# Optimization experiments

Hardware: AMD Instinct MI355X
Metric: run time of the kernel (lower is better)

The kernel has to match this reference:

```python
import jax, jax.numpy as jnp
import numpy as np

M_MARGIN = 0.5
S_SCALE = 30.0
EPS = 1e-12

def _l2norm(a):
    return a / jnp.maximum(jnp.linalg.norm(a, axis=1, keepdims=True), EPS)

def setup_inputs() -> dict:
    key = jax.random.key(0)
    k1, k2, k3 = jax.random.split(key, 3)
    B, D, V = 2048, 512, 32000
    x = jax.random.normal(k1, (B, D), dtype=jnp.float32)
    # kaiming_normal_ on (V, D): std = sqrt(2 / D)
    W = jax.random.normal(k2, (V, D), dtype=jnp.float32) * np.sqrt(2.0 / D)
    labels = jax.random.randint(k3, (B,), 0, V, dtype=jnp.int64)
    return {"x": x, "W": W, "labels": labels}

def reference(x, W, labels):
    cos_m, sin_m = jnp.cos(M_MARGIN), jnp.sin(M_MARGIN)
    nx = _l2norm(x)            # [B, D]
    nW = _l2norm(W)            # [V, D]
    cosine = nx @ nW.T         # [B, V]
    B = cosine.shape[0]
    rows = jnp.arange(B)
    # phi only matters at the label column (phi.where(one_hot, cosine))
    cos_y = cosine[rows, labels]                            # [B]
    sin_y = jnp.sqrt(jnp.clip(1.0 - cos_y * cos_y, 0.0, 1.0))
    phi_y = cos_y * cos_m - sin_y * sin_m                   # [B]
    logits = cosine.at[rows, labels].set(phi_y) * S_SCALE   # [B, V]
    logp = jax.nn.log_softmax(logits, axis=1)
    return -logp[rows, labels].sum() / B
```

## Files before the change

### kernel.cpp

```cpp
#include <hip/hip_runtime.h>
#include <math.h>
#include <stdint.h>

#define B_ROWS 2048
#define D_DIM  512
#define V_COLS 32000
#define BM 128
#define BN 128
#define BK 64
#define KSTEPS (D_DIM / BK)
#define NCT    (V_COLS / BN)
#define S_SC   30.0f
#define COS_M  0.8775825618903728f
#define SIN_M  0.479425538604203f

typedef float f32x4 __attribute__((ext_vector_type(4)));
typedef long  i64x2 __attribute__((ext_vector_type(2)));

__device__ __forceinline__ void load16_to_lds(const void* g, void* l) {
  __builtin_amdgcn_global_load_lds(
      (__attribute__((address_space(1))) void*)(g),
      (__attribute__((address_space(3))) void*)(l),
      16, 0, 0);
}

__global__ void fused_norm_kernel(const float* __restrict__ x,
                                  const float* __restrict__ W,
                                  uint8_t* __restrict__ nx,
                                  uint8_t* __restrict__ nw,
                                  float* __restrict__ rowsum,
                                  float* __restrict__ out) {
  if (blockIdx.x == 0 && threadIdx.x == 0) out[0] = 0.f;
  if (blockIdx.x < B_ROWS / 256) rowsum[blockIdx.x * 256 + threadIdx.x] = 0.f;
  const int lane = threadIdx.x & 63;
  const int wave = threadIdx.x >> 6;
  const int gr   = blockIdx.x * 4 + wave;
  const float* src;
  uint8_t* dst;
  if (gr < B_ROWS) {
    src = x + (size_t)gr * D_DIM;
    dst = nx + (size_t)gr * D_DIM;
  } else {
    src = W + (size_t)(gr - B_ROWS) * D_DIM;
    dst = nw + (size_t)(gr - B_ROWS) * D_DIM;
  }
  const float4* r4 = (const float4*)src;
  float4 v0 = r4[2 * lane];
  float4 v1 = r4[2 * lane + 1];
  float ss = v0.x*v0.x + v0.y*v0.y + v0.z*v0.z + v0.w*v0.w
           + v1.x*v1.x + v1.y*v1.y + v1.z*v1.z + v1.w*v1.w;
  #pragma unroll
  for (int off = 32; off >= 1; off >>= 1) ss += __shfl_xor(ss, off, 64);
  float inv = 1.0f / fmaxf(sqrtf(ss), 1e-12f);
  int p0 = __builtin_amdgcn_cvt_pk_fp8_f32(v0.x * inv, v0.y * inv, 0, false);
  p0     = __builtin_amdgcn_cvt_pk_fp8_f32(v0.z * inv, v0.w * inv, p0, true);
  int p1 = __builtin_amdgcn_cvt_pk_fp8_f32(v1.x * inv, v1.y * inv, 0, false);
  p1     = __builtin_amdgcn_cvt_pk_fp8_f32(v1.z * inv, v1.w * inv, p1, true);
  ((int2*)dst)[lane] = make_int2(p0, p1);
}

__global__ __launch_bounds__(256, 4)
void arc_gemm_kernel(const uint8_t* __restrict__ nx,
                     const uint8_t* __restrict__ nw,
                     const int* __restrict__ labels,
                     float* __restrict__ rowsum,
                     float* __restrict__ lbl_logit) {
  __shared__ uint8_t sA[2][BM * BK];
  __shared__ uint8_t sB[2][BN * BK];

  const int id = blockIdx.x;
  const int ct = ((id >> 7) << 3) | (id & 7);
  if (ct >= NCT) return;
  const int rt = (id >> 3) & 15;
  const int m0 = rt * BM;
  const int n0 = ct * BN;

  const int tid  = threadIdx.x;
  const int wave = tid >> 6;
  const int lane = tid & 63;
  const int wm   = wave >> 1;
  const int wn   = wave & 1;
  const int quad = lane >> 4;
  const int l16  = lane & 15;

  const int srow = tid >> 2;
  const int jg   = (tid & 3) ^ ((srow >> 1) & 3);
  const uint8_t* gA = nx + (size_t)(m0 + srow) * D_DIM + jg * 16;
  const uint8_t* gB = nw + (size_t)(n0 + srow) * D_DIM + jg * 16;
  const int ldsOff0 = wave * 1024;
  const int ldsOff1 = 4096 + wave * 1024;

  const int cSlot = (quad ^ ((l16 >> 1) & 3)) << 4;
  const int aBase = (wm * 64 + l16) * BK + cSlot;
  const int bBase = (wn * 64 + l16) * BK + cSlot;

  f32x4 acc[4][4];
  #pragma unroll
  for (int i = 0; i < 4; ++i)
    #pragma unroll
    for (int j = 0; j < 4; ++j) acc[i][j] = (f32x4){0.f, 0.f, 0.f, 0.f};

  load16_to_lds(gA,              &sA[0][ldsOff0]);
  load16_to_lds(gA + 64 * D_DIM, &sA[0][ldsOff1]);
  load16_to_lds(gB,              &sB[0][ldsOff0]);
  load16_to_lds(gB + 64 * D_DIM, &sB[0][ldsOff1]);

  #pragma unroll
  for (int ks = 0; ks < KSTEPS; ++ks) {
    __syncthreads();
    if (ks + 1 < KSTEPS) {
      const int off = (ks + 1) * BK;
      const int nb  = (ks + 1) & 1;
      load16_to_lds(gA + off,              &sA[nb][ldsOff0]);
      load16_to_lds(gA + 64 * D_DIM + off, &sA[nb][ldsOff1]);
      load16_to_lds(gB + off,              &sB[nb][ldsOff0]);
      load16_to_lds(gB + 64 * D_DIM + off, &sB[nb][ldsOff1]);
    }
    __syncthreads();

    const uint8_t* bA = sA[ks & 1];
    const uint8_t* bB = sB[ks & 1];
    i64x2 a2[4];
    #pragma unroll
    for (int mi = 0; mi < 4; ++mi)
      a2[mi] = *(const i64x2*)(bA + aBase + mi * 16 * BK);
    #pragma unroll
    for (int ni = 0; ni < 4; ++ni) {
      const i64x2 b2 = *(const i64x2*)(bB + bBase + ni * 16 * BK);
      #pragma unroll
      for (int mi = 0; mi < 4; ++mi) {
        acc[mi][ni] = __builtin_amdgcn_mfma_f32_16x16x32_fp8_fp8(a2[mi][0], b2[0], acc[mi][ni], 0, 0, 0);
        acc[mi][ni] = __builtin_amdgcn_mfma_f32_16x16x32_fp8_fp8(a2[mi][1], b2[1], acc[mi][ni], 0, 0, 0);
      }
    }
  }

  const int lblv = labels[m0 + wm * 64 + lane];
  #pragma unroll
  for (int mi = 0; mi < 4; ++mi) {
    #pragma unroll
    for (int r = 0; r < 4; ++r) {
      const int rw   = mi * 16 + quad * 4 + r;
      const int grow = m0 + wm * 64 + rw;
      const int lbl  = __shfl(lblv, rw, 64);
      float rsum = 0.f;
      #pragma unroll
      for (int ni = 0; ni < 4; ++ni) {
        float c = acc[mi][ni][r];
        const int gcol = n0 + wn * 64 + ni * 16 + l16;
        if (gcol == lbl) {
          float sy  = sqrtf(fminf(1.f, fmaxf(0.f, 1.f - c * c)));
          float phi = c * COS_M - sy * SIN_M;
          lbl_logit[grow] = S_SC * phi;
          c = phi;
        }
        rsum += __expf(S_SC * c - 30.0f);
      }
      #pragma unroll
      for (int off = 1; off < 16; off <<= 1)
        rsum += __shfl_xor(rsum, off, 64);
      if (l16 == 0) atomicAdd(&rowsum[grow], rsum);
    }
  }
}

__global__ void arc_finish_kernel(const float* __restrict__ rowsum,
                                  const float* __restrict__ lbl_logit,
                                  float* __restrict__ out) {
  const int row  = blockIdx.x * 256 + threadIdx.x;
  const int lane = threadIdx.x & 63;
  const int wave = threadIdx.x >> 6;
  float v = (30.0f + logf(rowsum[row]) - lbl_logit[row]) * (1.0f / (float)B_ROWS);
  #pragma unroll
  for (int off = 32; off >= 1; off >>= 1) v += __shfl_xor(v, off, 64);
  __shared__ float wsum[4];
  if (lane == 0) wsum[wave] = v;
  __syncthreads();
  if (threadIdx.x == 0) atomicAdd(out, wsum[0] + wsum[1] + wsum[2] + wsum[3]);
}

extern "C" void kernel_launch(void* const* d_in, const int* in_sizes, int n_in,
                              void* d_out, int out_size, void* d_ws, size_t ws_size,
                              hipStream_t stream) {
  const float* x      = (const float*)d_in[0];
  const float* W      = (const float*)d_in[1];
  const int*   labels = (const int*)d_in[2];
  float* out = (float*)d_out;

  char* ws = (char*)d_ws;
  uint8_t* nx = (uint8_t*)ws;
  uint8_t* nw = (uint8_t*)(ws + (size_t)B_ROWS * D_DIM);
  char* p = ws + (size_t)B_ROWS * D_DIM + (size_t)V_COLS * D_DIM;
  float* rowsum    = (float*)p;  p += (size_t)B_ROWS * 4;
  float* lbl_logit = (float*)p;

  hipLaunchKernelGGL(fused_norm_kernel, dim3((B_ROWS + V_COLS) / 4), dim3(256), 0, stream,
                     x, W, nx, nw, rowsum, out);
  hipLaunchKernelGGL(arc_gemm_kernel, dim3(32 * 16 * 8), dim3(256), 0, stream,
                     nx, nw, labels, rowsum, lbl_logit);
  hipLaunchKernelGGL(arc_finish_kernel, dim3(B_ROWS / 256), dim3(256), 0, stream,
                     rowsum, lbl_logit, out);
}
```

Measured before the change: 175.2 us.

## Enlarge GEMM tiles to 256x256 with 8 waves and triple-buffered LDS pipeline

Doubles the block tile to 256x256 with 512 threads (2x4 waves, each computing 128x64), which raises operand reuse per LDS byte. It replaces the double-buffer scheme, which had two barriers per k-step, with a three-stage buffer that uses explicit vmcnt waits and a single barrier, plus setprio around the MFMA block. Block-to-tile mapping is also remapped so that consecutive blocks share column tiles. The costs are higher register pressure (32 accumulators per wave), 96KB of LDS, and fewer blocks (1000), which risks worse tail balance across CUs.

```diff
diff --git a/kernel.cpp b/kernel.cpp
--- a/kernel.cpp
+++ b/kernel.cpp
@@ -5,10 +5,11 @@
 #define B_ROWS 2048
 #define D_DIM  512
 #define V_COLS 32000
-#define BM 128
-#define BN 128
+#define BM 256
+#define BN 256
 #define BK 64
 #define KSTEPS (D_DIM / BK)
+#define NRT    (B_ROWS / BM)
 #define NCT    (V_COLS / BN)
 #define S_SC   30.0f
 #define COS_M  0.8775825618903728f
@@ -59,27 +60,25 @@
   ((int2*)dst)[lane] = make_int2(p0, p1);
 }
 
-__global__ __launch_bounds__(256, 4)
+__global__ __launch_bounds__(512, 2)
 void arc_gemm_kernel(const uint8_t* __restrict__ nx,
                      const uint8_t* __restrict__ nw,
                      const int* __restrict__ labels,
                      float* __restrict__ rowsum,
                      float* __restrict__ lbl_logit) {
-  __shared__ uint8_t sA[2][BM * BK];
-  __shared__ uint8_t sB[2][BN * BK];
+  __shared__ uint8_t sA[3][BM * BK];
+  __shared__ uint8_t sB[3][BN * BK];
 
   const int id = blockIdx.x;
-  const int ct = ((id >> 7) << 3) | (id & 7);
-  if (ct >= NCT) return;
-  const int rt = (id >> 3) & 15;
-  const int m0 = rt * BM;
-  const int n0 = ct * BN;
+  const int wg = (id & 7) * NCT + (id >> 3);
+  const int m0 = (wg & (NRT - 1)) * BM;
+  const int n0 = (wg >> 3) * BN;
 
   const int tid  = threadIdx.x;
   const int wave = tid >> 6;
   const int lane = tid & 63;
-  const int wm   = wave >> 1;
-  const int wn   = wave & 1;
+  const int wm   = wave >> 2;
+  const int wn   = wave & 3;
   const int quad = lane >> 4;
   const int l16  = lane & 15;
 
@@ -87,62 +86,69 @@
   const int jg   = (tid & 3) ^ ((srow >> 1) & 3);
   const uint8_t* gA = nx + (size_t)(m0 + srow) * D_DIM + jg * 16;
   const uint8_t* gB = nw + (size_t)(n0 + srow) * D_DIM + jg * 16;
-  const int ldsOff0 = wave * 1024;
-  const int ldsOff1 = 4096 + wave * 1024;
+  const int ldsW = wave * 1024;
 
   const int cSlot = (quad ^ ((l16 >> 1) & 3)) << 4;
-  const int aBase = (wm * 64 + l16) * BK + cSlot;
-  const int bBase = (wn * 64 + l16) * BK + cSlot;
-
-  f32x4 acc[4][4];
-  #pragma unroll
-  for (int i = 0; i < 4; ++i)
+  const int aBase = (wm * 128 + l16) * BK + cSlot;
+  const int bBase = (wn * 64  + l16) * BK + cSlot;
+
+  f32x4 acc[8][4];
+  #pragma unroll
+  for (int i = 0; i < 8; ++i)
     #pragma unroll
     for (int j = 0; j < 4; ++j) acc[i][j] = (f32x4){0.f, 0.f, 0.f, 0.f};
 
-  load16_to_lds(gA,              &sA[0][ldsOff0]);
-  load16_to_lds(gA + 64 * D_DIM, &sA[0][ldsOff1]);
-  load16_to_lds(gB,              &sB[0][ldsOff0]);
-  load16_to_lds(gB + 64 * D_DIM, &sB[0][ldsOff1]);
-
-  #pragma unroll
-  for (int ks = 0; ks < KSTEPS; ++ks) {
-    __syncthreads();
-    if (ks + 1 < KSTEPS) {
-      const int off = (ks + 1) * BK;
-      const int nb  = (ks + 1) & 1;
-      load16_to_lds(gA + off,              &sA[nb][ldsOff0]);
-      load16_to_lds(gA + 64 * D_DIM + off, &sA[nb][ldsOff1]);
-      load16_to_lds(gB + off,              &sB[nb][ldsOff0]);
-      load16_to_lds(gB + 64 * D_DIM + off, &sB[nb][ldsOff1]);
-    }
-    __syncthreads();
-
-    const uint8_t* bA = sA[ks & 1];
-    const uint8_t* bB = sB[ks & 1];
-    i64x2 a2[4];
-    #pragma unroll
-    for (int mi = 0; mi < 4; ++mi)
-      a2[mi] = *(const i64x2*)(bA + aBase + mi * 16 * BK);
+#define STAGE(buf, t) do {                                        \
+    const int _o = (t) * BK;                                      \
+    load16_to_lds(gA + _o,               &sA[(buf)][ldsW]);       \
+    load16_to_lds(gA + 128 * D_DIM + _o, &sA[(buf)][8192 + ldsW]);\
+    load16_to_lds(gB + _o,               &sB[(buf)][ldsW]);       \
+    load16_to_lds(gB + 128 * D_DIM + _o, &sB[(buf)][8192 + ldsW]);\
+  } while (0)
+
+  STAGE(0, 0);
+  STAGE(1, 1);
+
+  #pragma unroll
+  for (int t = 0; t < KSTEPS; ++t) {
+    if (t < KSTEPS - 1) asm volatile("s_waitcnt vmcnt(4)" ::: "memory");
+    else                asm volatile("s_waitcnt vmcnt(0)" ::: "memory");
+    __builtin_amdgcn_s_barrier();
+    __builtin_amdgcn_sched_barrier(0);
+    if (t + 2 < KSTEPS) STAGE((t + 2) % 3, t + 2);
+    __builtin_amdgcn_sched_barrier(0);
+
+    const uint8_t* bA = sA[t % 3];
+    const uint8_t* bB = sB[t % 3];
+    i64x2 a2[8];
+    #pragma unroll
+    for (int mi = 0; mi < 8; ++mi)
+      a2[mi] = *(const i64x2*)(bA + aBase + mi * 1024);
+    __builtin_amdgcn_s_setprio(1);
     #pragma unroll
     for (int ni = 0; ni < 4; ++ni) {
-      const i64x2 b2 = *(const i64x2*)(bB + bBase + ni * 16 * BK);
+      const i64x2 b2 = *(const i64x2*)(bB + bBase + ni * 1024);
       #pragma unroll
-      for (int mi = 0; mi < 4; ++mi) {
+      for (int mi = 0; mi < 8; ++mi) {
         acc[mi][ni] = __builtin_amdgcn_mfma_f32_16x16x32_fp8_fp8(a2[mi][0], b2[0], acc[mi][ni], 0, 0, 0);
         acc[mi][ni] = __builtin_amdgcn_mfma_f32_16x16x32_fp8_fp8(a2[mi][1], b2[1], acc[mi][ni], 0, 0, 0);
       }
     }
+    __builtin_amdgcn_s_setprio(0);
   }
-
-  const int lblv = labels[m0 + wm * 64 + lane];
-  #pragma unroll
-  for (int mi = 0; mi < 4; ++mi) {
+#undef STAGE
+
+  const int rowbase = m0 + wm * 128;
+  const int lblv0 = labels[rowbase + lane];
+  const int lblv1 = labels[rowbase + 64 + lane];
+  #pragma unroll
+  for (int mi = 0; mi < 8; ++mi) {
     #pragma unroll
     for (int r = 0; r < 4; ++r) {
       const int rw   = mi * 16 + quad * 4 + r;
-      const int grow = m0 + wm * 64 + rw;
-      const int lbl  = __shfl(lblv, rw, 64);
+      const int grow = rowbase + rw;
+      const int lbl  = __shfl(mi < 4 ? lblv0 : lblv1,
+                              (mi & 3) * 16 + quad * 4 + r, 64);
       float rsum = 0.f;
       #pragma unroll
       for (int ni = 0; ni < 4; ++ni) {
@@ -196,7 +202,7 @@
 
   hipLaunchKernelGGL(fused_norm_kernel, dim3((B_ROWS + V_COLS) / 4), dim3(256), 0, stream,
                      x, W, nx, nw, rowsum, out);
-  hipLaunchKernelGGL(arc_gemm_kernel, dim3(32 * 16 * 8), dim3(256), 0, stream,
+  hipLaunchKernelGGL(arc_gemm_kernel, dim3(NRT * NCT), dim3(512), 0, stream,
                      nx, nw, labels, rowsum, lbl_logit);
   hipLaunchKernelGGL(arc_finish_kernel, dim3(B_ROWS / 256), dim3(256), 0, stream,
                      rowsum, lbl_logit, out);
```

Result: slower. 222.3 us (+26.9%).

## Fuse norm, GEMM and finish into one persistent cooperative kernel with grid syncs

Applied to the files above, without the earlier changes.

Replaces three kernel launches with a single cooperative persistent kernel of 512 blocks. Each block grid-strides over the normalization rows and over the GEMM tiles, with grid-wide barriers between the phases, and finishes with the loss reduction. This removes launch gaps and inter-kernel drain and fill. It adds grid-sync overhead and fixes the GEMM to 512 resident blocks, which may leave little latency hiding and cause tail imbalance over the 2000 tiles. The normalization load pattern also changes to coalesced float4 loads at lane and lane+64.

```diff
diff --git a/kernel.cpp b/kernel.cpp
--- a/kernel.cpp
+++ b/kernel.cpp
@@ -1,4 +1,5 @@
 #include <hip/hip_runtime.h>
+#include <hip/hip_cooperative_groups.h>
 #include <math.h>
 #include <stdint.h>
 
@@ -10,6 +11,8 @@
 #define BK 64
 #define KSTEPS (D_DIM / BK)
 #define NCT    (V_COLS / BN)
+#define GRID   512
+#define NIDS   4096
 #define S_SC   30.0f
 #define COS_M  0.8775825618903728f
 #define SIN_M  0.479425538604203f
@@ -24,159 +27,157 @@
       16, 0, 0);
 }
 
-__global__ void fused_norm_kernel(const float* __restrict__ x,
-                                  const float* __restrict__ W,
-                                  uint8_t* __restrict__ nx,
-                                  uint8_t* __restrict__ nw,
-                                  float* __restrict__ rowsum,
-                                  float* __restrict__ out) {
-  if (blockIdx.x == 0 && threadIdx.x == 0) out[0] = 0.f;
-  if (blockIdx.x < B_ROWS / 256) rowsum[blockIdx.x * 256 + threadIdx.x] = 0.f;
-  const int lane = threadIdx.x & 63;
-  const int wave = threadIdx.x >> 6;
-  const int gr   = blockIdx.x * 4 + wave;
-  const float* src;
-  uint8_t* dst;
-  if (gr < B_ROWS) {
-    src = x + (size_t)gr * D_DIM;
-    dst = nx + (size_t)gr * D_DIM;
-  } else {
-    src = W + (size_t)(gr - B_ROWS) * D_DIM;
-    dst = nw + (size_t)(gr - B_ROWS) * D_DIM;
-  }
-  const float4* r4 = (const float4*)src;
-  float4 v0 = r4[2 * lane];
-  float4 v1 = r4[2 * lane + 1];
-  float ss = v0.x*v0.x + v0.y*v0.y + v0.z*v0.z + v0.w*v0.w
-           + v1.x*v1.x + v1.y*v1.y + v1.z*v1.z + v1.w*v1.w;
-  #pragma unroll
-  for (int off = 32; off >= 1; off >>= 1) ss += __shfl_xor(ss, off, 64);
-  float inv = 1.0f / fmaxf(sqrtf(ss), 1e-12f);
-  int p0 = __builtin_amdgcn_cvt_pk_fp8_f32(v0.x * inv, v0.y * inv, 0, false);
-  p0     = __builtin_amdgcn_cvt_pk_fp8_f32(v0.z * inv, v0.w * inv, p0, true);
-  int p1 = __builtin_amdgcn_cvt_pk_fp8_f32(v1.x * inv, v1.y * inv, 0, false);
-  p1     = __builtin_amdgcn_cvt_pk_fp8_f32(v1.z * inv, v1.w * inv, p1, true);
-  ((int2*)dst)[lane] = make_int2(p0, p1);
-}
-
 __global__ __launch_bounds__(256, 4)
-void arc_gemm_kernel(const uint8_t* __restrict__ nx,
-                     const uint8_t* __restrict__ nw,
-                     const int* __restrict__ labels,
-                     float* __restrict__ rowsum,
-                     float* __restrict__ lbl_logit) {
+void arc_fused_kernel(const float* __restrict__ x,
+                      const float* __restrict__ W,
+                      const int* __restrict__ labels,
+                      uint8_t* __restrict__ nx,
+                      uint8_t* __restrict__ nw,
+                      float* __restrict__ rowsum,
+                      float* __restrict__ lbl_logit,
+                      float* __restrict__ out) {
   __shared__ uint8_t sA[2][BM * BK];
   __shared__ uint8_t sB[2][BN * BK];
 
-  const int id = blockIdx.x;
-  const int ct = ((id >> 7) << 3) | (id & 7);
-  if (ct >= NCT) return;
-  const int rt = (id >> 3) & 15;
-  const int m0 = rt * BM;
-  const int n0 = ct * BN;
-
   const int tid  = threadIdx.x;
+  const int lane = tid & 63;
   const int wave = tid >> 6;
-  const int lane = tid & 63;
+
+  if (blockIdx.x == 0 && tid == 0) out[0] = 0.f;
+  if (blockIdx.x < B_ROWS / 256) rowsum[blockIdx.x * 256 + tid] = 0.f;
+
+  for (int r = blockIdx.x * 4 + wave; r < B_ROWS + V_COLS; r += GRID * 4) {
+    const float* src;
+    uint8_t* dst;
+    if (r < B_ROWS) {
+      src = x + (size_t)r * D_DIM;
+      dst = nx + (size_t)r * D_DIM;
+    } else {
+      src = W + (size_t)(r - B_ROWS) * D_DIM;
+      dst = nw + (size_t)(r - B_ROWS) * D_DIM;
+    }
+    const float4* r4 = (const float4*)src;
+    float4 v0 = r4[lane];
+    float4 v1 = r4[lane + 64];
+    float ss = v0.x*v0.x + v0.y*v0.y + v0.z*v0.z + v0.w*v0.w
+             + v1.x*v1.x + v1.y*v1.y + v1.z*v1.z + v1.w*v1.w;
+    #pragma unroll
+    for (int off = 32; off >= 1; off >>= 1) ss += __shfl_xor(ss, off, 64);
+    float inv = 1.0f / fmaxf(sqrtf(ss), 1e-12f);
+    int p0 = __builtin_amdgcn_cvt_pk_fp8_f32(v0.x * inv, v0.y * inv, 0, false);
+    p0     = __builtin_amdgcn_cvt_pk_fp8_f32(v0.z * inv, v0.w * inv, p0, true);
+    int p1 = __builtin_amdgcn_cvt_pk_fp8_f32(v1.x * inv, v1.y * inv, 0, false);
+    p1     = __builtin_amdgcn_cvt_pk_fp8_f32(v1.z * inv, v1.w * inv, p1, true);
+    ((int*)dst)[lane]      = p0;
+    ((int*)dst)[64 + lane] = p1;
+  }
+
+  cooperative_groups::this_grid().sync();
+
   const int wm   = wave >> 1;
   const int wn   = wave & 1;
   const int quad = lane >> 4;
   const int l16  = lane & 15;
-
   const int srow = tid >> 2;
   const int jg   = (tid & 3) ^ ((srow >> 1) & 3);
-  const uint8_t* gA = nx + (size_t)(m0 + srow) * D_DIM + jg * 16;
-  const uint8_t* gB = nw + (size_t)(n0 + srow) * D_DIM + jg * 16;
   const int ldsOff0 = wave * 1024;
   const int ldsOff1 = 4096 + wave * 1024;
-
   const int cSlot = (quad ^ ((l16 >> 1) & 3)) << 4;
   const int aBase = (wm * 64 + l16) * BK + cSlot;
   const int bBase = (wn * 64 + l16) * BK + cSlot;
 
-  f32x4 acc[4][4];
-  #pragma unroll
-  for (int i = 0; i < 4; ++i)
-    #pragma unroll
-    for (int j = 0; j < 4; ++j) acc[i][j] = (f32x4){0.f, 0.f, 0.f, 0.f};
-
-  load16_to_lds(gA,              &sA[0][ldsOff0]);
-  load16_to_lds(gA + 64 * D_DIM, &sA[0][ldsOff1]);
-  load16_to_lds(gB,              &sB[0][ldsOff0]);
-  load16_to_lds(gB + 64 * D_DIM, &sB[0][ldsOff1]);
-
-  #pragma unroll
-  for (int ks = 0; ks < KSTEPS; ++ks) {
-    __syncthreads();
-    if (ks + 1 < KSTEPS) {
-      const int off = (ks + 1) * BK;
-      const int nb  = (ks + 1) & 1;
-      load16_to_lds(gA + off,              &sA[nb][ldsOff0]);
-      load16_to_lds(gA + 64 * D_DIM + off, &sA[nb][ldsOff1]);
-      load16_to_lds(gB + off,              &sB[nb][ldsOff0]);
-      load16_to_lds(gB + 64 * D_DIM + off, &sB[nb][ldsOff1]);
+  for (int v = blockIdx.x; v < NIDS; v += GRID) {
+    const int ct = ((v >> 7) << 3) | (v & 7);
+    if (ct >= NCT) continue;
+    const int rt = (v >> 3) & 15;
+    const int m0 = rt * BM;
+    const int n0 = ct * BN;
+
+    const uint8_t* gA = nx + (size_t)(m0 + srow) * D_DIM + jg * 16;
+    const uint8_t* gB = nw + (size_t)(n0 + srow) * D_DIM + jg * 16;
+
+    f32x4 acc[4][4];
+    #pragma unroll
+    for (int i = 0; i < 4; ++i)
+      #pragma unroll
+      for (int j = 0; j < 4; ++j) acc[i][j] = (f32x4){0.f, 0.f, 0.f, 0.f};
+
+    load16_to_lds(gA,              &sA[0][ldsOff0]);
+    load16_to_lds(gA + 64 * D_DIM, &sA[0][ldsOff1]);
+    load16_to_lds(gB,              &sB[0][ldsOff0]);
+    load16_to_lds(gB + 64 * D_DIM, &sB[0][ldsOff1]);
+
+    #pragma unroll
+    for (int ks = 0; ks < KSTEPS; ++ks) {
+      __syncthreads();
+      if (ks + 1 < KSTEPS) {
+        const int off = (ks + 1) * BK;
+        const int nb  = (ks + 1) & 1;
+        load16_to_lds(gA + off,              &sA[nb][ldsOff0]);
+        load16_to_lds(gA + 64 * D_DIM + off, &sA[nb][ldsOff1]);
+        load16_to_lds(gB + off,              &sB[nb][ldsOff0]);
+        load16_to_lds(gB + 64 * D_DIM + off, &sB[nb][ldsOff1]);
+      }
+      __syncthreads();
+
+      const uint8_t* bA = sA[ks & 1];
+      const uint8_t* bB = sB[ks & 1];
+      i64x2 a2[4];
+      #pragma unroll
+      for (int mi = 0; mi < 4; ++mi)
+        a2[mi] = *(const i64x2*)(bA + aBase + mi * 16 * BK);
+      #pragma unroll
+      for (int ni = 0; ni < 4; ++ni) {
+        const i64x2 b2 = *(const i64x2*)(bB + bBase + ni * 16 * BK);
+        #pragma unroll
+        for (int mi = 0; mi < 4; ++mi) {
+          acc[mi][ni] = __builtin_amdgcn_mfma_f32_16x16x32_fp8_fp8(a2[mi][0], b2[0], acc[mi][ni], 0, 0, 0);
+          acc[mi][ni] = __builtin_amdgcn_mfma_f32_16x16x32_fp8_fp8(a2[mi][1], b2[1], acc[mi][ni], 0, 0, 0);
+        }
+      }
     }
-    __syncthreads();
-
-    const uint8_t* bA = sA[ks & 1];
-    const uint8_t* bB = sB[ks & 1];
-    i64x2 a2[4];
-    #pragma unroll
-    for (int mi = 0; mi < 4; ++mi)
-      a2[mi] = *(const i64x2*)(bA + aBase + mi * 16 * BK);
-    #pragma unroll
-    for (int ni = 0; ni < 4; ++ni) {
-      const i64x2 b2 = *(const i64x2*)(bB + bBase + ni * 16 * BK);
-      #pragma unroll
-      for (int mi = 0; mi < 4; ++mi) {
-        acc[mi][ni] = __builtin_amdgcn_mfma_f32_16x16x32_fp8_fp8(a2[mi][0], b2[0], acc[mi][ni], 0, 0, 0);
-        acc[mi][ni] = __builtin_amdgcn_mfma_f32_16x16x32_fp8_fp8(a2[mi][1], b2[1], acc[mi][ni], 0, 0, 0);
+
+    const int lblv = labels[m0 + wm * 64 + lane];
+    #pragma unroll
+    for (int mi = 0; mi < 4; ++mi) {
+      #pragma unroll
+      for (int r = 0; r < 4; ++r) {
+        const int rw   = mi * 16 + quad * 4 + r;
+        const int grow = m0 + wm * 64 + rw;
+        const int lbl  = __shfl(lblv, rw, 64);
+        float rsum = 0.f;
+        #pragma unroll
+        for (int ni = 0; ni < 4; ++ni) {
+          float c = acc[mi][ni][r];
+          const int gcol = n0 + wn * 64 + ni * 16 + l16;
+          if (gcol == lbl) {
+            float sy  = sqrtf(fminf(1.f, fmaxf(0.f, 1.f - c * c)));
+            float phi = c * COS_M - sy * SIN_M;
+            lbl_logit[grow] = S_SC * phi;
+            c = phi;
+          }
+          rsum += __expf(S_SC * c - 30.0f);
+        }
+        #pragma unroll
+        for (int off = 1; off < 16; off <<= 1)
+          rsum += __shfl_xor(rsum, off, 64);
+        if (l16 == 0) atomicAdd(&rowsum[grow], rsum);
       }
     }
   }
 
-  const int lblv = labels[m0 + wm * 64 + lane];
-  #pragma unroll
-  for (int mi = 0; mi < 4; ++mi) {
-    #pragma unroll
-    for (int r = 0; r < 4; ++r) {
-      const int rw   = mi * 16 + quad * 4 + r;
-      const int grow = m0 + wm * 64 + rw;
-      const int lbl  = __shfl(lblv, rw, 64);
-      float rsum = 0.f;
-      #pragma unroll
-      for (int ni = 0; ni < 4; ++ni) {
-        float c = acc[mi][ni][r];
-        const int gcol = n0 + wn * 64 + ni * 16 + l16;
-        if (gcol == lbl) {
-          float sy  = sqrtf(fminf(1.f, fmaxf(0.f, 1.f - c * c)));
-          float phi = c * COS_M - sy * SIN_M;
-          lbl_logit[grow] = S_SC * phi;
-          c = phi;
-        }
-        rsum += __expf(S_SC * c - 30.0f);
-      }
-      #pragma unroll
-      for (int off = 1; off < 16; off <<= 1)
-        rsum += __shfl_xor(rsum, off, 64);
-      if (l16 == 0) atomicAdd(&rowsum[grow], rsum);
-    }
+  cooperative_groups::this_grid().sync();
+
+  if (blockIdx.x < B_ROWS / 256) {
+    const int row = blockIdx.x * 256 + tid;
+    float vv = (30.0f + logf(rowsum[row]) - lbl_logit[row]) * (1.0f / (float)B_ROWS);
+    #pragma unroll
+    for (int off = 32; off >= 1; off >>= 1) vv += __shfl_xor(vv, off, 64);
+    float* wsum = (float*)sA;
+    if (lane == 0) wsum[wave] = vv;
+    __syncthreads();
+    if (tid == 0) atomicAdd(out, wsum[0] + wsum[1] + wsum[2] + wsum[3]);
   }
-}
-
-__global__ void arc_finish_kernel(const float* __restrict__ rowsum,
-                                  const float* __restrict__ lbl_logit,
-                                  float* __restrict__ out) {
-  const int row  = blockIdx.x * 256 + threadIdx.x;
-  const int lane = threadIdx.x & 63;
-  const int wave = threadIdx.x >> 6;
-  float v = (30.0f + logf(rowsum[row]) - lbl_logit[row]) * (1.0f / (float)B_ROWS);
-  #pragma unroll
-  for (int off = 32; off >= 1; off >>= 1) v += __shfl_xor(v, off, 64);
-  __shared__ float wsum[4];
-  if (lane == 0) wsum[wave] = v;
-  __syncthreads();
-  if (threadIdx.x == 0) atomicAdd(out, wsum[0] + wsum[1] + wsum[2] + wsum[3]);
 }
 
 extern "C" void kernel_launch(void* const* d_in, const int* in_sizes, int n_in,
@@ -194,10 +195,8 @@
   float* rowsum    = (float*)p;  p += (size_t)B_ROWS * 4;
   float* lbl_logit = (float*)p;
 
-  hipLaunchKernelGGL(fused_norm_kernel, dim3((B_ROWS + V_COLS) / 4), dim3(256), 0, stream,
-                     x, W, nx, nw, rowsum, out);
-  hipLaunchKernelGGL(arc_gemm_kernel, dim3(32 * 16 * 8), dim3(256), 0, stream,
-                     nx, nw, labels, rowsum, lbl_logit);
-  hipLaunchKernelGGL(arc_finish_kernel, dim3(B_ROWS / 256), dim3(256), 0, stream,
-                     rowsum, lbl_logit, out);
+  void* args[] = {(void*)&x, (void*)&W, (void*)&labels, (void*)&nx, (void*)&nw,
+                  (void*)&rowsum, (void*)&lbl_logit, (void*)&out};
+  hipLaunchCooperativeKernel(reinterpret_cast<void*>(arc_fused_kernel),
+                             dim3(GRID), dim3(256), args, 0, stream);
 }
```

Result: slower. 339.6 us (+93.9%).

## Triple-buffer GEMM LDS stages with explicit vmcnt waits

Applied to the files above, without the earlier changes.

Converts the FP8 GEMM main loop from double to triple buffering, prefetching two K-steps ahead with direct-to-LDS loads. Partial s_waitcnt vmcnt counts let newer loads stay in flight while the current stage is consumed, with raw s_barrier and sched_barrier fencing. The goal is to hide more global-load latency. The cost is 48KB of LDS per block instead of 32KB, with launch bounds reduced from 4 to 3 blocks per CU, so occupancy may drop.

```diff
diff --git a/kernel.cpp b/kernel.cpp
--- a/kernel.cpp
+++ b/kernel.cpp
@@ -59,14 +59,14 @@
   ((int2*)dst)[lane] = make_int2(p0, p1);
 }
 
-__global__ __launch_bounds__(256, 4)
+__global__ __launch_bounds__(256, 3)
 void arc_gemm_kernel(const uint8_t* __restrict__ nx,
                      const uint8_t* __restrict__ nw,
                      const int* __restrict__ labels,
                      float* __restrict__ rowsum,
                      float* __restrict__ lbl_logit) {
-  __shared__ uint8_t sA[2][BM * BK];
-  __shared__ uint8_t sB[2][BN * BK];
+  __shared__ uint8_t sA[3][BM * BK];
+  __shared__ uint8_t sB[3][BN * BK];
 
   const int id = blockIdx.x;
   const int ct = ((id >> 7) << 3) | (id & 7);
@@ -100,26 +100,32 @@
     #pragma unroll
     for (int j = 0; j < 4; ++j) acc[i][j] = (f32x4){0.f, 0.f, 0.f, 0.f};
 
-  load16_to_lds(gA,              &sA[0][ldsOff0]);
-  load16_to_lds(gA + 64 * D_DIM, &sA[0][ldsOff1]);
-  load16_to_lds(gB,              &sB[0][ldsOff0]);
-  load16_to_lds(gB + 64 * D_DIM, &sB[0][ldsOff1]);
+#define STAGE(buf, t) do {                                        \
+    const int _o = (t) * BK;                                      \
+    load16_to_lds(gA + _o,              &sA[(buf)][ldsOff0]);     \
+    load16_to_lds(gA + 64 * D_DIM + _o, &sA[(buf)][ldsOff1]);     \
+    load16_to_lds(gB + _o,              &sB[(buf)][ldsOff0]);     \
+    load16_to_lds(gB + 64 * D_DIM + _o, &sB[(buf)][ldsOff1]);     \
+  } while (0)
+
+  STAGE(0, 0);
+  STAGE(1, 1);
 
   #pragma unroll
   for (int ks = 0; ks < KSTEPS; ++ks) {
-    __syncthreads();
-    if (ks + 1 < KSTEPS) {
-      const int off = (ks + 1) * BK;
-      const int nb  = (ks + 1) & 1;
-      load16_to_lds(gA + off,              &sA[nb][ldsOff0]);
-      load16_to_lds(gA + 64 * D_DIM + off, &sA[nb][ldsOff1]);
-      load16_to_lds(gB + off,              &sB[nb][ldsOff0]);
-      load16_to_lds(gB + 64 * D_DIM + off, &sB[nb][ldsOff1]);
-    }
-    __syncthreads();
-
-    const uint8_t* bA = sA[ks & 1];
-    const uint8_t* bB = sB[ks & 1];
+    __builtin_amdgcn_sched_barrier(0);
+    __builtin_amdgcn_s_barrier();
+    __builtin_amdgcn_sched_barrier(0);
+    if (ks + 2 < KSTEPS) STAGE((ks + 2) % 3, ks + 2);
+    if (ks < KSTEPS - 2)       asm volatile("s_waitcnt vmcnt(8)" ::: "memory");
+    else if (ks == KSTEPS - 2) asm volatile("s_waitcnt vmcnt(4)" ::: "memory");
+    else                       asm volatile("s_waitcnt vmcnt(0)" ::: "memory");
+    __builtin_amdgcn_sched_barrier(0);
+    __builtin_amdgcn_s_barrier();
+    __builtin_amdgcn_sched_barrier(0);
+
+    const uint8_t* bA = sA[ks % 3];
+    const uint8_t* bB = sB[ks % 3];
     i64x2 a2[4];
     #pragma unroll
     for (int mi = 0; mi < 4; ++mi)
@@ -134,6 +140,7 @@
       }
     }
   }
+#undef STAGE
 
   const int lblv = labels[m0 + wm * 64 + lane];
   #pragma unroll
```

Result: no change. 176.8 us (+0.9%).
